# Kernel tuning notes

Hardware: AMD Instinct MI355X
Metric: run time of the kernel (lower is better)

## Reference

```python
import jax, jax.numpy as jnp
import numpy as np

TOKENS, DIM, N_EXPERTS, TOPK = 8192, 4096, 256, 8

def setup_inputs() -> dict:
    key = jax.random.key(0)
    k1, k2 = jax.random.split(key)
    x = jax.random.normal(k1, (TOKENS, DIM), dtype=jnp.float32)
    weight = jax.random.normal(k2, (N_EXPERTS, DIM), dtype=jnp.float32) * (DIM ** -0.5)
    return {"x": x, "weight": weight}

def reference(x, weight):
    # logits: [tokens, n_experts]
    logits = jnp.einsum('td,ed->te', x, weight)
    scores = jax.nn.sigmoid(logits)
    topv, indices = jax.lax.top_k(scores, TOPK)          # [tokens, topk]
    gates = topv / jnp.sum(topv, axis=-1, keepdims=True)
    return gates, indices
```

## Files before the change

### kernel.cpp

```cpp
#include <hip/hip_runtime.h>
#include <hip/hip_bf16.h>
#include <hip/hip_fp16.h>
#include <math.h>

#define TOKENS   8192
#define DIM      4096
#define NEXP     256
#define TOPK     8
#define CAND     12

#define MT   32
#define BK   64
#define LDH  72

typedef _Float16 f16x8 __attribute__((ext_vector_type(8)));
typedef _Float16 f16x4 __attribute__((ext_vector_type(4)));
typedef float    f32x4 __attribute__((ext_vector_type(4)));

__global__ __launch_bounds__(256)
void convert_w(const float* __restrict__ w, _Float16* __restrict__ wh) {
    const int t = blockIdx.x * 256 + threadIdx.x;
    const float4* wp = (const float4*)w;
    f16x8* op = (f16x8*)wh;
    #pragma unroll
    for (int i = 0; i < 2; ++i) {
        const int o = i * 65536 + t;
        const float4 a = wp[2 * o];
        const float4 b = wp[2 * o + 1];
        f16x8 h;
        h[0] = (_Float16)a.x; h[1] = (_Float16)a.y;
        h[2] = (_Float16)a.z; h[3] = (_Float16)a.w;
        h[4] = (_Float16)b.x; h[5] = (_Float16)b.y;
        h[6] = (_Float16)b.z; h[7] = (_Float16)b.w;
        op[o] = h;
    }
}

__global__ __launch_bounds__(512)
void gemm_fp16(const float* __restrict__ x, const _Float16* __restrict__ wh,
               float* __restrict__ logits, int kspan) {
    __shared__ _Float16 ah[MT][LDH];
    __shared__ _Float16 bh[NEXP][LDH];

    const int t    = threadIdx.x;
    const int wave = t >> 6, lane = t & 63;
    const int m0   = blockIdx.x * MT;
    const int kb   = blockIdx.y * kspan;
    float* lp      = logits + (size_t)blockIdx.y * TOKENS * NEXP;

    const int wr   = (wave >> 2) * 16;
    const int wc   = (wave & 3) * 64;

    const int ar = t >> 4, ak = (t & 15) * 4;
    const int br = t >> 3, bk = (t & 7) * 8;

    const int fm = lane & 15;
    const int fk = (lane >> 4) * 8;

    f32x4 acc[4];
    #pragma unroll
    for (int nt = 0; nt < 4; ++nt) acc[nt] = (f32x4){0.f, 0.f, 0.f, 0.f};

    float4 xa = *(const float4*)(x + (size_t)(m0 + ar) * DIM + kb + ak);
    f16x8 wb[4];
    #pragma unroll
    for (int c = 0; c < 4; ++c)
        wb[c] = *(const f16x8*)(wh + (size_t)(c * 64 + br) * DIM + kb + bk);

    for (int k0 = kb; k0 < kb + kspan; k0 += BK) {
        f16x4 hx;
        hx[0] = (_Float16)xa.x; hx[1] = (_Float16)xa.y;
        hx[2] = (_Float16)xa.z; hx[3] = (_Float16)xa.w;
        *(f16x4*)&ah[ar][ak] = hx;
        #pragma unroll
        for (int c = 0; c < 4; ++c)
            *(f16x8*)&bh[c * 64 + br][bk] = wb[c];
        __syncthreads();

        if (k0 + BK < kb + kspan) {
            xa = *(const float4*)(x + (size_t)(m0 + ar) * DIM + k0 + BK + ak);
            #pragma unroll
            for (int c = 0; c < 4; ++c)
                wb[c] = *(const f16x8*)(wh + (size_t)(c * 64 + br) * DIM + k0 + BK + bk);
        }

        #pragma unroll
        for (int kk = 0; kk < 2; ++kk) {
            const f16x8 af = *(const f16x8*)&ah[wr + fm][kk * 32 + fk];
            #pragma unroll
            for (int nt = 0; nt < 4; ++nt) {
                const f16x8 bf = *(const f16x8*)&bh[wc + nt * 16 + fm][kk * 32 + fk];
                acc[nt] = __builtin_amdgcn_mfma_f32_16x16x32_f16(af, bf, acc[nt], 0, 0, 0);
            }
        }
        __syncthreads();
    }

    #pragma unroll
    for (int nt = 0; nt < 4; ++nt) {
        #pragma unroll
        for (int r = 0; r < 4; ++r) {
            const int m = m0 + wr + (lane >> 4) * 4 + r;
            const int n = wc + nt * 16 + (lane & 15);
            lp[(size_t)m * NEXP + n] = acc[nt][r];
        }
    }
}

__global__ __launch_bounds__(256)
void topk_cand(const float* __restrict__ logits, int* __restrict__ cand,
               int nsplit) {
    const int lane  = threadIdx.x & 63;
    const int token = blockIdx.x * 4 + (threadIdx.x >> 6);
    const float* lp = logits + (size_t)token * NEXP;

    float s[4];
    #pragma unroll
    for (int j = 0; j < 4; ++j) s[j] = 0.f;
    for (int p = 0; p < nsplit; ++p) {
        const float* pp = lp + (size_t)p * TOKENS * NEXP;
        #pragma unroll
        for (int j = 0; j < 4; ++j) s[j] += pp[j * 64 + lane];
    }

    int mye = 0;
    #pragma unroll
    for (int r = 0; r < CAND; ++r) {
        float bv = s[0];
        int   be = lane;
        #pragma unroll
        for (int j = 1; j < 4; ++j) {
            if (s[j] > bv) { bv = s[j]; be = j * 64 + lane; }
        }
        #pragma unroll
        for (int off = 32; off > 0; off >>= 1) {
            const float ov = __shfl_xor(bv, off, 64);
            const int   oe = __shfl_xor(be, off, 64);
            if (ov > bv || (ov == bv && oe < be)) { bv = ov; be = oe; }
        }
        if (lane == r) mye = be;
        if ((be & 63) == lane) s[be >> 6] = -1e30f;
    }

    if (lane < CAND) cand[token * CAND + lane] = mye;
}

__global__ __launch_bounds__(256)
void rescore(const float* __restrict__ x, const float* __restrict__ w,
             const int* __restrict__ cand, float* __restrict__ out) {
    const int wave = threadIdx.x >> 6, lane = threadIdx.x & 63;
    const int token = blockIdx.x * 4 + wave;

    const float4* xp4 = (const float4*)(x + (size_t)token * DIM);

    int ce[CAND];
    #pragma unroll
    for (int c = 0; c < CAND; ++c) ce[c] = cand[token * CAND + c];

    double tot[CAND];

    #pragma unroll
    for (int g = 0; g < 3; ++g) {
        const float4* wp0 = (const float4*)(w + (size_t)ce[g * 4 + 0] * DIM);
        const float4* wp1 = (const float4*)(w + (size_t)ce[g * 4 + 1] * DIM);
        const float4* wp2 = (const float4*)(w + (size_t)ce[g * 4 + 2] * DIM);
        const float4* wp3 = (const float4*)(w + (size_t)ce[g * 4 + 3] * DIM);

        double a0x=0,a0y=0,a0z=0,a0w=0, a1x=0,a1y=0,a1z=0,a1w=0;
        double a2x=0,a2y=0,a2z=0,a2w=0, a3x=0,a3y=0,a3z=0,a3w=0;

        #pragma unroll 4
        for (int i = 0; i < 16; ++i) {
            const int o = lane + i * 64;
            const float4 xv = xp4[o];
            const float4 w0 = wp0[o];
            const float4 w1 = wp1[o];
            const float4 w2 = wp2[o];
            const float4 w3 = wp3[o];
            a0x = fma((double)xv.x, (double)w0.x, a0x);
            a0y = fma((double)xv.y, (double)w0.y, a0y);
            a0z = fma((double)xv.z, (double)w0.z, a0z);
            a0w = fma((double)xv.w, (double)w0.w, a0w);
            a1x = fma((double)xv.x, (double)w1.x, a1x);
            a1y = fma((double)xv.y, (double)w1.y, a1y);
            a1z = fma((double)xv.z, (double)w1.z, a1z);
            a1w = fma((double)xv.w, (double)w1.w, a1w);
            a2x = fma((double)xv.x, (double)w2.x, a2x);
            a2y = fma((double)xv.y, (double)w2.y, a2y);
            a2z = fma((double)xv.z, (double)w2.z, a2z);
            a2w = fma((double)xv.w, (double)w2.w, a2w);
            a3x = fma((double)xv.x, (double)w3.x, a3x);
            a3y = fma((double)xv.y, (double)w3.y, a3y);
            a3z = fma((double)xv.z, (double)w3.z, a3z);
            a3w = fma((double)xv.w, (double)w3.w, a3w);
        }
        tot[g * 4 + 0] = (a0x + a0y) + (a0z + a0w);
        tot[g * 4 + 1] = (a1x + a1y) + (a1z + a1w);
        tot[g * 4 + 2] = (a2x + a2y) + (a2z + a2w);
        tot[g * 4 + 3] = (a3x + a3y) + (a3z + a3w);
    }

    #pragma unroll
    for (int off = 32; off > 0; off >>= 1) {
        #pragma unroll
        for (int c = 0; c < CAND; ++c)
            tot[c] += __shfl_xor(tot[c], off, 64);
    }

    int rank[CAND];
    #pragma unroll
    for (int c = 0; c < CAND; ++c) {
        int r = 0;
        #pragma unroll
        for (int j = 0; j < CAND; ++j) {
            if (j == c) continue;
            if (tot[j] > tot[c] || (tot[j] == tot[c] && ce[j] < ce[c])) ++r;
        }
        rank[c] = r;
    }

    float sig[CAND];
    float sum = 0.f;
    #pragma unroll
    for (int c = 0; c < CAND; ++c) {
        sig[c] = 1.0f / (1.0f + expf(-(float)tot[c]));
        if (rank[c] < TOPK) sum += sig[c];
    }

    if (lane < TOPK) {
        float g = 0.f; int ei = 0;
        #pragma unroll
        for (int c = 0; c < CAND; ++c)
            if (rank[c] == lane) { g = sig[c]; ei = ce[c]; }
        out[(size_t)token * TOPK + lane] = g / sum;
        out[(size_t)TOKENS * TOPK + (size_t)token * TOPK + lane] = (float)ei;
    }
}

extern "C" void kernel_launch(void* const* d_in, const int* in_sizes, int n_in,
                              void* d_out, int out_size, void* d_ws, size_t ws_size,
                              hipStream_t stream) {
    const float* x = (const float*)d_in[0];
    const float* w = (const float*)d_in[1];
    float* out     = (float*)d_out;

    const size_t plane = (size_t)TOKENS * NEXP * sizeof(float);
    const size_t fixed = (size_t)TOKENS * CAND * sizeof(int)
                       + (size_t)NEXP * DIM * sizeof(_Float16);
    int S = 4;
    if (ws_size < 4 * plane + fixed) S = (ws_size >= 2 * plane + fixed) ? 2 : 1;

    float*     logits = (float*)d_ws;
    int*       candp  = (int*)((char*)d_ws + (size_t)S * plane);
    _Float16*  wh     = (_Float16*)((char*)candp + (size_t)TOKENS * CAND * sizeof(int));

    convert_w<<<256, 256, 0, stream>>>(w, wh);
    dim3 ggrid(TOKENS / MT, S);
    gemm_fp16<<<ggrid, 512, 0, stream>>>(x, wh, logits, DIM / S);
    topk_cand<<<TOKENS / 4, 256, 0, stream>>>(logits, candp, S);
    rescore<<<TOKENS / 4, 256, 0, stream>>>(x, w, candp, out);
}
```

Baseline: 381.2 us.

## Use 128-row GEMM tiles with pre-swizzled fp16 weights and direct global-to-LDS loads

The weight conversion kernel now writes fp16 weights in an MFMA-fragment-swizzled tile layout. The GEMM uses 128-token tiles with a 4x4 MFMA block per wave, and loads the weight tiles straight into LDS with global_load_lds. This raises per-block data reuse and cuts redundant weight traffic relative to the old 32-row tiles. The rescore kernel also merges its 12 candidate dot products into one pass over x, with wave-uniform candidate indices via readfirstlane, which adds register pressure from 24 double accumulators.

Measured after the change: 358.4 us. -6.0%, faster.

```diff
diff --git a/kernel.cpp b/kernel.cpp
--- a/kernel.cpp
+++ b/kernel.cpp
@@ -9,100 +9,128 @@
 #define TOPK     8
 #define CAND     12
 
-#define MT   32
-#define BK   64
-#define LDH  72
+#define MT3      128
+#define BK3      64
+#define KG       (DIM / 32)
 
 typedef _Float16 f16x8 __attribute__((ext_vector_type(8)));
 typedef _Float16 f16x4 __attribute__((ext_vector_type(4)));
 typedef float    f32x4 __attribute__((ext_vector_type(4)));
 
+typedef const __attribute__((address_space(1))) unsigned int* gas_ptr;
+typedef       __attribute__((address_space(3))) unsigned int* las_ptr;
+
 __global__ __launch_bounds__(256)
-void convert_w(const float* __restrict__ w, _Float16* __restrict__ wh) {
-    const int t = blockIdx.x * 256 + threadIdx.x;
-    const float4* wp = (const float4*)w;
-    f16x8* op = (f16x8*)wh;
-    #pragma unroll
-    for (int i = 0; i < 2; ++i) {
-        const int o = i * 65536 + t;
-        const float4 a = wp[2 * o];
-        const float4 b = wp[2 * o + 1];
-        f16x8 h;
-        h[0] = (_Float16)a.x; h[1] = (_Float16)a.y;
-        h[2] = (_Float16)a.z; h[3] = (_Float16)a.w;
-        h[4] = (_Float16)b.x; h[5] = (_Float16)b.y;
-        h[6] = (_Float16)b.z; h[7] = (_Float16)b.w;
-        op[o] = h;
-    }
-}
-
-__global__ __launch_bounds__(512)
-void gemm_fp16(const float* __restrict__ x, const _Float16* __restrict__ wh,
-               float* __restrict__ logits, int kspan) {
-    __shared__ _Float16 ah[MT][LDH];
-    __shared__ _Float16 bh[NEXP][LDH];
-
-    const int t    = threadIdx.x;
-    const int wave = t >> 6, lane = t & 63;
-    const int m0   = blockIdx.x * MT;
-    const int kb   = blockIdx.y * kspan;
-    float* lp      = logits + (size_t)blockIdx.y * TOKENS * NEXP;
-
-    const int wr   = (wave >> 2) * 16;
-    const int wc   = (wave & 3) * 64;
-
-    const int ar = t >> 4, ak = (t & 15) * 4;
-    const int br = t >> 3, bk = (t & 7) * 8;
-
-    const int fm = lane & 15;
-    const int fk = (lane >> 4) * 8;
-
-    f32x4 acc[4];
-    #pragma unroll
-    for (int nt = 0; nt < 4; ++nt) acc[nt] = (f32x4){0.f, 0.f, 0.f, 0.f};
-
-    float4 xa = *(const float4*)(x + (size_t)(m0 + ar) * DIM + kb + ak);
-    f16x8 wb[4];
-    #pragma unroll
-    for (int c = 0; c < 4; ++c)
-        wb[c] = *(const f16x8*)(wh + (size_t)(c * 64 + br) * DIM + kb + bk);
-
-    for (int k0 = kb; k0 < kb + kspan; k0 += BK) {
-        f16x4 hx;
-        hx[0] = (_Float16)xa.x; hx[1] = (_Float16)xa.y;
-        hx[2] = (_Float16)xa.z; hx[3] = (_Float16)xa.w;
-        *(f16x4*)&ah[ar][ak] = hx;
-        #pragma unroll
-        for (int c = 0; c < 4; ++c)
-            *(f16x8*)&bh[c * 64 + br][bk] = wb[c];
+void convert_w(const float* __restrict__ w, _Float16* __restrict__ whs) {
+    const int g = blockIdx.x * 256 + threadIdx.x;
+    const int tile = g >> 6, c = g & 63;
+    const int q = c >> 4, r = c & 15;
+    const int ng = tile / KG, kg = tile % KG;
+    const int n = ng * 16 + r, k = kg * 32 + q * 8;
+    const float4 a = *(const float4*)(w + (size_t)n * DIM + k);
+    const float4 b = *(const float4*)(w + (size_t)n * DIM + k + 4);
+    f16x8 h;
+    h[0] = (_Float16)a.x; h[1] = (_Float16)a.y;
+    h[2] = (_Float16)a.z; h[3] = (_Float16)a.w;
+    h[4] = (_Float16)b.x; h[5] = (_Float16)b.y;
+    h[6] = (_Float16)b.z; h[7] = (_Float16)b.w;
+    *(f16x8*)(whs + (size_t)g * 8) = h;
+}
+
+__global__ __launch_bounds__(512, 2)
+void gemm_v3(const float* __restrict__ x, const _Float16* __restrict__ whs,
+             float* __restrict__ logits, int kspan) {
+    __shared__ _Float16 As[16 * 512];
+    __shared__ _Float16 Bs[32 * 512];
+
+    const int t = threadIdx.x, w = t >> 6, lane = t & 63;
+    const int m0 = blockIdx.x * MT3;
+    const int kb = blockIdx.y * kspan;
+    float* lp    = logits + (size_t)blockIdx.y * TOKENS * NEXP;
+
+    const int rg = w >> 2;
+    const int cg = w & 3;
+
+    const int am  = t >> 2;
+    const int ack = (t & 3) * 2;
+    const int amg = am >> 4, amr = am & 15;
+    const int aoff0 = ((amg * 2 + (ack >> 2)) * 64 + (ack & 3) * 16 + amr) * 8;
+    const int ack1  = ack + 1;
+    const int aoff1 = ((amg * 2 + (ack1 >> 2)) * 64 + (ack1 & 3) * 16 + amr) * 8;
+
+    f32x4 acc[4][4];
+    #pragma unroll
+    for (int i = 0; i < 4; ++i)
+        #pragma unroll
+        for (int j = 0; j < 4; ++j) acc[i][j] = (f32x4){0.f, 0.f, 0.f, 0.f};
+
+    const float* xrow = x + (size_t)(m0 + am) * DIM + ack * 8;
+    float4 xr0 = *(const float4*)(xrow + kb);
+    float4 xr1 = *(const float4*)(xrow + kb + 4);
+    float4 xr2 = *(const float4*)(xrow + kb + 8);
+    float4 xr3 = *(const float4*)(xrow + kb + 12);
+
+    for (int k0 = kb; k0 < kb + kspan; k0 += BK3) {
+        #pragma unroll
+        for (int c = 0; c < 4; ++c) {
+            const int ti  = w * 4 + c;
+            const int ng  = ti >> 1, kgl = ti & 1;
+            const _Float16* gp = whs + ((size_t)(ng * KG + (k0 >> 5) + kgl)) * 512
+                                     + lane * 8;
+            __builtin_amdgcn_global_load_lds((gas_ptr)gp, (las_ptr)&Bs[ti * 512],
+                                             16, 0, 0);
+        }
+        {
+            f16x8 h0, h1;
+            h0[0] = (_Float16)xr0.x; h0[1] = (_Float16)xr0.y;
+            h0[2] = (_Float16)xr0.z; h0[3] = (_Float16)xr0.w;
+            h0[4] = (_Float16)xr1.x; h0[5] = (_Float16)xr1.y;
+            h0[6] = (_Float16)xr1.z; h0[7] = (_Float16)xr1.w;
+            h1[0] = (_Float16)xr2.x; h1[1] = (_Float16)xr2.y;
+            h1[2] = (_Float16)xr2.z; h1[3] = (_Float16)xr2.w;
+            h1[4] = (_Float16)xr3.x; h1[5] = (_Float16)xr3.y;
+            h1[6] = (_Float16)xr3.z; h1[7] = (_Float16)xr3.w;
+            *(f16x8*)&As[aoff0] = h0;
+            *(f16x8*)&As[aoff1] = h1;
+        }
         __syncthreads();
 
-        if (k0 + BK < kb + kspan) {
-            xa = *(const float4*)(x + (size_t)(m0 + ar) * DIM + k0 + BK + ak);
-            #pragma unroll
-            for (int c = 0; c < 4; ++c)
-                wb[c] = *(const f16x8*)(wh + (size_t)(c * 64 + br) * DIM + k0 + BK + bk);
+        if (k0 + BK3 < kb + kspan) {
+            xr0 = *(const float4*)(xrow + k0 + BK3);
+            xr1 = *(const float4*)(xrow + k0 + BK3 + 4);
+            xr2 = *(const float4*)(xrow + k0 + BK3 + 8);
+            xr3 = *(const float4*)(xrow + k0 + BK3 + 12);
         }
 
         #pragma unroll
         for (int kk = 0; kk < 2; ++kk) {
-            const f16x8 af = *(const f16x8*)&ah[wr + fm][kk * 32 + fk];
-            #pragma unroll
-            for (int nt = 0; nt < 4; ++nt) {
-                const f16x8 bf = *(const f16x8*)&bh[wc + nt * 16 + fm][kk * 32 + fk];
-                acc[nt] = __builtin_amdgcn_mfma_f32_16x16x32_f16(af, bf, acc[nt], 0, 0, 0);
+            f16x8 af[4], bf[4];
+            #pragma unroll
+            for (int mt = 0; mt < 4; ++mt)
+                af[mt] = *(const f16x8*)&As[(((rg * 4 + mt) * 2 + kk) * 64 + lane) * 8];
+            #pragma unroll
+            for (int nt = 0; nt < 4; ++nt)
+                bf[nt] = *(const f16x8*)&Bs[(((cg * 4 + nt) * 2 + kk) * 64 + lane) * 8];
+            #pragma unroll
+            for (int mt = 0; mt < 4; ++mt)
+                #pragma unroll
+                for (int nt = 0; nt < 4; ++nt)
+                    acc[mt][nt] = __builtin_amdgcn_mfma_f32_16x16x32_f16(
+                        af[mt], bf[nt], acc[mt][nt], 0, 0, 0);
+        }
+        __syncthreads();
+    }
+
+    #pragma unroll
+    for (int mt = 0; mt < 4; ++mt) {
+        #pragma unroll
+        for (int nt = 0; nt < 4; ++nt) {
+            #pragma unroll
+            for (int r = 0; r < 4; ++r) {
+                const int m = m0 + (rg * 4 + mt) * 16 + (lane >> 4) * 4 + r;
+                const int n = (cg * 4 + nt) * 16 + (lane & 15);
+                lp[(size_t)m * NEXP + n] = acc[mt][nt][r];
             }
-        }
-        __syncthreads();
-    }
-
-    #pragma unroll
-    for (int nt = 0; nt < 4; ++nt) {
-        #pragma unroll
-        for (int r = 0; r < 4; ++r) {
-            const int m = m0 + wr + (lane >> 4) * 4 + r;
-            const int n = wc + nt * 16 + (lane & 15);
-            lp[(size_t)m * NEXP + n] = acc[nt][r];
         }
     }
 }
@@ -154,51 +182,36 @@
     const float4* xp4 = (const float4*)(x + (size_t)token * DIM);
 
     int ce[CAND];
-    #pragma unroll
-    for (int c = 0; c < CAND; ++c) ce[c] = cand[token * CAND + c];
+    const float4* wp[CAND];
+    #pragma unroll
+    for (int c = 0; c < CAND; ++c) {
+        ce[c] = __builtin_amdgcn_readfirstlane(cand[token * CAND + c]);
+        wp[c] = (const float4*)(w + (size_t)ce[c] * DIM);
+    }
+
+    double acc[2 * CAND];
+    #pragma unroll
+    for (int c = 0; c < 2 * CAND; ++c) acc[c] = 0.0;
+
+    #pragma unroll 2
+    for (int i = 0; i < 16; ++i) {
+        const int o = lane + i * 64;
+        const float4 xv = xp4[o];
+        const double dx = (double)xv.x, dy = (double)xv.y;
+        const double dz = (double)xv.z, dw = (double)xv.w;
+        #pragma unroll
+        for (int c = 0; c < CAND; ++c) {
+            const float4 wv = wp[c][o];
+            double e = fma(dx, (double)wv.x, acc[2 * c]);
+            acc[2 * c] = fma(dy, (double)wv.y, e);
+            double f = fma(dz, (double)wv.z, acc[2 * c + 1]);
+            acc[2 * c + 1] = fma(dw, (double)wv.w, f);
+        }
+    }
 
     double tot[CAND];
-
-    #pragma unroll
-    for (int g = 0; g < 3; ++g) {
-        const float4* wp0 = (const float4*)(w + (size_t)ce[g * 4 + 0] * DIM);
-        const float4* wp1 = (const float4*)(w + (size_t)ce[g * 4 + 1] * DIM);
-        const float4* wp2 = (const float4*)(w + (size_t)ce[g * 4 + 2] * DIM);
-        const float4* wp3 = (const float4*)(w + (size_t)ce[g * 4 + 3] * DIM);
-
-        double a0x=0,a0y=0,a0z=0,a0w=0, a1x=0,a1y=0,a1z=0,a1w=0;
-        double a2x=0,a2y=0,a2z=0,a2w=0, a3x=0,a3y=0,a3z=0,a3w=0;
-
-        #pragma unroll 4
-        for (int i = 0; i < 16; ++i) {
-            const int o = lane + i * 64;
-            const float4 xv = xp4[o];
-            const float4 w0 = wp0[o];
-            const float4 w1 = wp1[o];
-            const float4 w2 = wp2[o];
-            const float4 w3 = wp3[o];
-            a0x = fma((double)xv.x, (double)w0.x, a0x);
-            a0y = fma((double)xv.y, (double)w0.y, a0y);
-            a0z = fma((double)xv.z, (double)w0.z, a0z);
-            a0w = fma((double)xv.w, (double)w0.w, a0w);
-            a1x = fma((double)xv.x, (double)w1.x, a1x);
-            a1y = fma((double)xv.y, (double)w1.y, a1y);
-            a1z = fma((double)xv.z, (double)w1.z, a1z);
-            a1w = fma((double)xv.w, (double)w1.w, a1w);
-            a2x = fma((double)xv.x, (double)w2.x, a2x);
-            a2y = fma((double)xv.y, (double)w2.y, a2y);
-            a2z = fma((double)xv.z, (double)w2.z, a2z);
-            a2w = fma((double)xv.w, (double)w2.w, a2w);
-            a3x = fma((double)xv.x, (double)w3.x, a3x);
-            a3y = fma((double)xv.y, (double)w3.y, a3y);
-            a3z = fma((double)xv.z, (double)w3.z, a3z);
-            a3w = fma((double)xv.w, (double)w3.w, a3w);
-        }
-        tot[g * 4 + 0] = (a0x + a0y) + (a0z + a0w);
-        tot[g * 4 + 1] = (a1x + a1y) + (a1z + a1w);
-        tot[g * 4 + 2] = (a2x + a2y) + (a2z + a2w);
-        tot[g * 4 + 3] = (a3x + a3y) + (a3z + a3w);
-    }
+    #pragma unroll
+    for (int c = 0; c < CAND; ++c) tot[c] = acc[2 * c] + acc[2 * c + 1];
 
     #pragma unroll
     for (int off = 32; off > 0; off >>= 1) {
@@ -252,11 +265,11 @@
 
     float*     logits = (float*)d_ws;
     int*       candp  = (int*)((char*)d_ws + (size_t)S * plane);
-    _Float16*  wh     = (_Float16*)((char*)candp + (size_t)TOKENS * CAND * sizeof(int));
-
-    convert_w<<<256, 256, 0, stream>>>(w, wh);
-    dim3 ggrid(TOKENS / MT, S);
-    gemm_fp16<<<ggrid, 512, 0, stream>>>(x, wh, logits, DIM / S);
+    _Float16*  whs    = (_Float16*)((char*)candp + (size_t)TOKENS * CAND * sizeof(int));
+
+    convert_w<<<512, 256, 0, stream>>>(w, whs);
+    dim3 ggrid(TOKENS / MT3, S);
+    gemm_v3<<<ggrid, 512, 0, stream>>>(x, whs, logits, DIM / S);
     topk_cand<<<TOKENS / 4, 256, 0, stream>>>(logits, candp, S);
     rescore<<<TOKENS / 4, 256, 0, stream>>>(x, w, candp, out);
 }
```
